# Kernel optimization log

Measured on AMD Instinct MI355X. Metric: run time of the kernel, lower is better.

The kernel has to match this reference:

```python
import jax, jax.numpy as jnp
import numpy as np

N = 50000       # nodes
E = 800000      # edges
IN = 128        # in_channels
HID = 64        # hidden_channels
OUT = 32        # out_channels
H = 4           # heads
EH = 64         # edge_hidden_channels
EOUT = 2        # edge_out_channels
NEG_SLOPE = 0.2 # PyG GATConv default


def gat_conv(x, edge_index, W, att_src, att_dst, bias, num_nodes):
    """PyG GATConv, concat=False, add_self_loops=False, eval mode (no dropout).
    edge_attr is ignored because edge_dim=None (lin_edge is None in PyG).
    Returns (out [N, C], alpha [E, H])."""
    heads, C = att_src.shape
    xl = (x @ W).reshape(-1, heads, C)                 # [N, H, C]
    src, dst = edge_index[0], edge_index[1]
    a_src = jnp.sum(xl * att_src, axis=-1)             # [N, H]
    a_dst = jnp.sum(xl * att_dst, axis=-1)             # [N, H]
    alpha = jax.nn.leaky_relu(a_src[src] + a_dst[dst], NEG_SLOPE)  # [E, H]
    # segment softmax over destination nodes
    amax = jax.ops.segment_max(alpha, dst, num_segments=num_nodes)
    amax = jnp.where(jnp.isfinite(amax), amax, 0.0)
    ex = jnp.exp(alpha - amax[dst])
    denom = jax.ops.segment_sum(ex, dst, num_segments=num_nodes)
    alpha_n = ex / (denom[dst] + 1e-16)                # [E, H]
    msg = xl[src] * alpha_n[:, :, None]                # [E, H, C]
    out = jax.ops.segment_sum(msg, dst, num_segments=num_nodes)  # [N, H, C]
    out = out.mean(axis=1) + bias                      # concat=False -> head mean
    return out, alpha_n


def setup_inputs() -> dict:
    key = jax.random.key(0)
    ks = jax.random.split(key, 16)
    x = jax.random.normal(ks[0], (N, IN), dtype=jnp.float32)
    edge_index = jax.random.randint(ks[1], (2, E), 0, N, dtype=jnp.int32)
    edge_attr = jax.random.normal(ks[2], (E, 5), dtype=jnp.float32)
    s = lambda fan: 1.0 / np.sqrt(fan)
    W1 = jax.random.normal(ks[3], (IN, H * HID), dtype=jnp.float32) * s(IN)
    att1_src = jax.random.normal(ks[4], (H, HID), dtype=jnp.float32) * s(HID)
    att1_dst = jax.random.normal(ks[5], (H, HID), dtype=jnp.float32) * s(HID)
    b1 = jnp.zeros((HID,), dtype=jnp.float32)
    W3 = jax.random.normal(ks[6], (HID, H * OUT), dtype=jnp.float32) * s(HID)
    att3_src = jax.random.normal(ks[7], (H, OUT), dtype=jnp.float32) * s(OUT)
    att3_dst = jax.random.normal(ks[8], (H, OUT), dtype=jnp.float32) * s(OUT)
    b3 = jnp.zeros((OUT,), dtype=jnp.float32)
    EIN = 2 * OUT + H  # cat(out_src, alpha, out_dst)
    mW1 = jax.random.normal(ks[9], (EIN, EH), dtype=jnp.float32) * s(EIN)
    mb1 = jnp.zeros((EH,), dtype=jnp.float32)
    mW2 = jax.random.normal(ks[10], (EH, EOUT), dtype=jnp.float32) * s(EH)
    mb2 = jnp.zeros((EOUT,), dtype=jnp.float32)
    return {"x": x, "edge_index": edge_index, "edge_attr": edge_attr,
            "return_attention_weights": 1,
            "W1": W1, "att1_src": att1_src, "att1_dst": att1_dst, "b1": b1,
            "W3": W3, "att3_src": att3_src, "att3_dst": att3_dst, "b3": b3,
            "mW1": mW1, "mb1": mb1, "mW2": mW2, "mb2": mb2}


def reference(x, edge_index, edge_attr, return_attention_weights,
              W1, att1_src, att1_dst, b1, W3, att3_src, att3_dst, b3,
              mW1, mb1, mW2, mb2):
    edge_len = edge_attr.shape[0]  # == E (no self loops added)
    out, alpha = gat_conv(x, edge_index, W1, att1_src, att1_dst, b1, N)
    out, alpha = gat_conv(out, edge_index, W3, att3_src, att3_dst, b3, N)
    # F.dropout with training=False is the identity (eval mode)
    ei = edge_index[:, :edge_len]
    al = alpha[:edge_len, :]
    out_src = out[ei[0]]                                # [E, OUT]
    out_dst = out[ei[1]]                                # [E, OUT]
    edge_feat = jnp.concatenate([out_src, al, out_dst], axis=-1)  # [E, 2*OUT+H]
    h = jax.nn.relu(edge_feat @ mW1 + mb1)
    edge_out = h @ mW2 + mb2                            # [E, EOUT]
    return (out, edge_out)
```

## Files before the change

### kernel.cpp

```cpp
#include <hip/hip_runtime.h>
#include <hip/hip_fp16.h>

constexpr int NN   = 50000;
constexpr int EE   = 800000;
constexpr int INF  = 128;
constexpr int NH   = 4;
constexpr int GR64 = (NN + 63) / 64;
constexpr int EB   = (EE + 255) / 256;
constexpr int NCH  = (NN + 255) / 256;

struct __align__(8) h4 { __half2 a, b; };

__device__ __forceinline__ float elw(float a) {
    a = (a > 0.f) ? a : 0.2f * a;
    return __expf(a);
}


template <int CH, bool HOUT>
__device__ __forceinline__ void gemm_att_tile48(const float* __restrict__ A,
                                                const float* __restrict__ B,
                                                void* __restrict__ Cv,
                                                const float* __restrict__ att_s,
                                                const float* __restrict__ att_d,
                                                float* __restrict__ a_s,
                                                float* __restrict__ a_d,
                                                int N, int K, int M,
                                                int row0, int col0, int tid,
                                                float (*As)[68], float (*Bs)[132]) {
    const int tx = tid & 15, ty = tid >> 4;
    float acc[4][8] = {};

    for (int k0 = 0; k0 < K; k0 += 32) {
        {
            const int a_row = tid >> 2;
            const int a_k   = (tid & 3) * 8;
            const int gr    = row0 + a_row;
            float4 v0 = make_float4(0.f,0.f,0.f,0.f), v1 = make_float4(0.f,0.f,0.f,0.f);
            if (gr < N) {
                const float* ap = A + (size_t)gr * K + k0 + a_k;
                v0 = *(const float4*)ap;
                v1 = *(const float4*)(ap + 4);
            }
            As[a_k + 0][a_row] = v0.x; As[a_k + 1][a_row] = v0.y;
            As[a_k + 2][a_row] = v0.z; As[a_k + 3][a_row] = v0.w;
            As[a_k + 4][a_row] = v1.x; As[a_k + 5][a_row] = v1.y;
            As[a_k + 6][a_row] = v1.z; As[a_k + 7][a_row] = v1.w;
        }
        {
            const int b_k = tid >> 4;
            const int b_c = (tid & 15) * 8;
            const float* bp0 = B + (size_t)(k0 + b_k) * M + col0 + b_c;
            const float* bp1 = B + (size_t)(k0 + b_k + 16) * M + col0 + b_c;
            *(float4*)&Bs[b_k][b_c]          = *(const float4*)bp0;
            *(float4*)&Bs[b_k][b_c + 4]      = *(const float4*)(bp0 + 4);
            *(float4*)&Bs[b_k + 16][b_c]     = *(const float4*)bp1;
            *(float4*)&Bs[b_k + 16][b_c + 4] = *(const float4*)(bp1 + 4);
        }
        __syncthreads();
        #pragma unroll
        for (int kk = 0; kk < 32; ++kk) {
            const float4 a  = *(const float4*)&As[kk][ty * 4];
            const float4 b0 = *(const float4*)&Bs[kk][tx * 4];
            const float4 b1 = *(const float4*)&Bs[kk][64 + tx * 4];
            const float av[4] = {a.x, a.y, a.z, a.w};
            const float bv[8] = {b0.x,b0.y,b0.z,b0.w,b1.x,b1.y,b1.z,b1.w};
            #pragma unroll
            for (int i = 0; i < 4; ++i)
                #pragma unroll
                for (int j = 0; j < 8; ++j)
                    acc[i][j] = fmaf(av[i], bv[j], acc[i][j]);
        }
        __syncthreads();
    }

    const int c0 = col0 + tx * 4;
    const int c1 = c0 + 64;
    const int head0 = c0 / CH, pos0 = c0 % CH;
    const int head1 = c1 / CH, pos1 = c1 % CH;
    float attS[8], attD[8];
    #pragma unroll
    for (int j = 0; j < 4; ++j) {
        attS[j]     = att_s[head0 * CH + pos0 + j];
        attD[j]     = att_d[head0 * CH + pos0 + j];
        attS[j + 4] = att_s[head1 * CH + pos1 + j];
        attD[j + 4] = att_d[head1 * CH + pos1 + j];
    }
    #pragma unroll
    for (int i = 0; i < 4; ++i) {
        const int r = row0 + ty * 4 + i;
        if (r < N) {
            if constexpr (HOUT) {
                __half* C = (__half*)Cv;
                __half* cp0 = C + (size_t)r * M + c0;
                __half* cp1 = C + (size_t)r * M + c1;
                *(__half2*)(cp0)     = __halves2half2(__float2half_rn(acc[i][0]), __float2half_rn(acc[i][1]));
                *(__half2*)(cp0 + 2) = __halves2half2(__float2half_rn(acc[i][2]), __float2half_rn(acc[i][3]));
                *(__half2*)(cp1)     = __halves2half2(__float2half_rn(acc[i][4]), __float2half_rn(acc[i][5]));
                *(__half2*)(cp1 + 2) = __halves2half2(__float2half_rn(acc[i][6]), __float2half_rn(acc[i][7]));
            } else {
                float* C = (float*)Cv;
                *(float4*)(C + (size_t)r * M + c0) = make_float4(acc[i][0], acc[i][1], acc[i][2], acc[i][3]);
                *(float4*)(C + (size_t)r * M + c1) = make_float4(acc[i][4], acc[i][5], acc[i][6], acc[i][7]);
            }
        }
        float ss0 = 0.f, sd0 = 0.f, ss1 = 0.f, sd1 = 0.f;
        #pragma unroll
        for (int j = 0; j < 4; ++j) {
            ss0 = fmaf(acc[i][j], attS[j], ss0);
            sd0 = fmaf(acc[i][j], attD[j], sd0);
            ss1 = fmaf(acc[i][j + 4], attS[j + 4], ss1);
            sd1 = fmaf(acc[i][j + 4], attD[j + 4], sd1);
        }
        #pragma unroll
        for (int msk = 1; msk < CH / 4; msk <<= 1) {
            ss0 += __shfl_xor(ss0, msk, 64);
            sd0 += __shfl_xor(sd0, msk, 64);
            ss1 += __shfl_xor(ss1, msk, 64);
            sd1 += __shfl_xor(sd1, msk, 64);
        }
        if ((tx & (CH / 4 - 1)) == 0 && r < N) {
            a_s[r * NH + head0] = ss0;
            a_d[r * NH + head0] = sd0;
            a_s[r * NH + head1] = ss1;
            a_d[r * NH + head1] = sd1;
        }
    }
}

__device__ __forceinline__ void gemm_pq_tile48(const float* __restrict__ A,
                                               const float* __restrict__ B,
                                               __half* __restrict__ C,
                                               int N, int K, int M,
                                               int row0, int col0, int tid,
                                               float (*As)[68], float (*Bs)[132]) {
    const int tx = tid & 15, ty = tid >> 4;
    float acc[4][8] = {};
    for (int k0 = 0; k0 < K; k0 += 32) {
        {
            const int a_row = tid >> 2;
            const int a_k   = (tid & 3) * 8;
            const int gr    = row0 + a_row;
            float4 v0 = make_float4(0.f,0.f,0.f,0.f), v1 = make_float4(0.f,0.f,0.f,0.f);
            if (gr < N) {
                const float* ap = A + (size_t)gr * K + k0 + a_k;
                v0 = *(const float4*)ap;
                v1 = *(const float4*)(ap + 4);
            }
            As[a_k + 0][a_row] = v0.x; As[a_k + 1][a_row] = v0.y;
            As[a_k + 2][a_row] = v0.z; As[a_k + 3][a_row] = v0.w;
            As[a_k + 4][a_row] = v1.x; As[a_k + 5][a_row] = v1.y;
            As[a_k + 6][a_row] = v1.z; As[a_k + 7][a_row] = v1.w;
        }
        {
            const int b_k = tid >> 4;
            const int b_c = (tid & 15) * 8;
            const float* bp0 = B + (size_t)(k0 + b_k) * M + col0 + b_c;
            const float* bp1 = B + (size_t)(k0 + b_k + 16) * M + col0 + b_c;
            *(float4*)&Bs[b_k][b_c]          = *(const float4*)bp0;
            *(float4*)&Bs[b_k][b_c + 4]      = *(const float4*)(bp0 + 4);
            *(float4*)&Bs[b_k + 16][b_c]     = *(const float4*)bp1;
            *(float4*)&Bs[b_k + 16][b_c + 4] = *(const float4*)(bp1 + 4);
        }
        __syncthreads();
        #pragma unroll
        for (int kk = 0; kk < 32; ++kk) {
            const float4 a  = *(const float4*)&As[kk][ty * 4];
            const float4 b0 = *(const float4*)&Bs[kk][tx * 4];
            const float4 b1 = *(const float4*)&Bs[kk][64 + tx * 4];
            const float av[4] = {a.x, a.y, a.z, a.w};
            const float bv[8] = {b0.x,b0.y,b0.z,b0.w,b1.x,b1.y,b1.z,b1.w};
            #pragma unroll
            for (int i = 0; i < 4; ++i)
                #pragma unroll
                for (int j = 0; j < 8; ++j)
                    acc[i][j] = fmaf(av[i], bv[j], acc[i][j]);
        }
        __syncthreads();
    }
    const int c0 = col0 + tx * 4;
    const int c1 = c0 + 64;
    #pragma unroll
    for (int i = 0; i < 4; ++i) {
        const int r = row0 + ty * 4 + i;
        if (r < N) {
            __half* cp0 = C + (size_t)r * M + c0;
            __half* cp1 = C + (size_t)r * M + c1;
            *(__half2*)(cp0)     = __halves2half2(__float2half_rn(acc[i][0]), __float2half_rn(acc[i][1]));
            *(__half2*)(cp0 + 2) = __halves2half2(__float2half_rn(acc[i][2]), __float2half_rn(acc[i][3]));
            *(__half2*)(cp1)     = __halves2half2(__float2half_rn(acc[i][4]), __float2half_rn(acc[i][5]));
            *(__half2*)(cp1 + 2) = __halves2half2(__float2half_rn(acc[i][6]), __float2half_rn(acc[i][7]));
        }
    }
}


__device__ __forceinline__ void softagg1_node(int n, int lane,
                                              const int* __restrict__ rowptr,
                                              const int* __restrict__ psrc,
                                              const float* __restrict__ a_s,
                                              const float* __restrict__ a_d,
                                              const __half* __restrict__ xl,
                                              const float* __restrict__ bias,
                                              float* __restrict__ out) {
    const int r0 = rowptr[n], r1 = rowptr[n + 1];
    const int hh = lane >> 4;
    const float ad = a_d[n * NH + hh];

    const h4* X = (const h4*)xl;
    float4 A0 = {0,0,0,0}, A1 = {0,0,0,0}, A2 = {0,0,0,0}, A3 = {0,0,0,0};
    float sum = 0.f;
    int j = r0;
    for (; j + 7 < r1; j += 8) {
        const int s0 = psrc[j],     s1 = psrc[j + 1], s2 = psrc[j + 2], s3 = psrc[j + 3];
        const int s4 = psrc[j + 4], s5 = psrc[j + 5], s6 = psrc[j + 6], s7 = psrc[j + 7];
        const float w0 = elw(a_s[s0 * NH + hh] + ad);
        const float w1 = elw(a_s[s1 * NH + hh] + ad);
        const float w2 = elw(a_s[s2 * NH + hh] + ad);
        const float w3 = elw(a_s[s3 * NH + hh] + ad);
        const float w4 = elw(a_s[s4 * NH + hh] + ad);
        const float w5 = elw(a_s[s5 * NH + hh] + ad);
        const float w6 = elw(a_s[s6 * NH + hh] + ad);
        const float w7 = elw(a_s[s7 * NH + hh] + ad);
        sum += ((w0 + w1) + (w2 + w3)) + ((w4 + w5) + (w6 + w7));
        const h4 v0 = X[(size_t)s0 * 64 + lane];
        const h4 v1 = X[(size_t)s1 * 64 + lane];
        const h4 v2 = X[(size_t)s2 * 64 + lane];
        const h4 v3 = X[(size_t)s3 * 64 + lane];
        const h4 v4 = X[(size_t)s4 * 64 + lane];
        const h4 v5 = X[(size_t)s5 * 64 + lane];
        const h4 v6 = X[(size_t)s6 * 64 + lane];
        const h4 v7 = X[(size_t)s7 * 64 + lane];
        float2 l0 = __half22float2(v0.a), m0 = __half22float2(v0.b);
        float2 l1 = __half22float2(v1.a), m1 = __half22float2(v1.b);
        float2 l2 = __half22float2(v2.a), m2 = __half22float2(v2.b);
        float2 l3 = __half22float2(v3.a), m3 = __half22float2(v3.b);
        float2 l4 = __half22float2(v4.a), m4 = __half22float2(v4.b);
        float2 l5 = __half22float2(v5.a), m5 = __half22float2(v5.b);
        float2 l6 = __half22float2(v6.a), m6 = __half22float2(v6.b);
        float2 l7 = __half22float2(v7.a), m7 = __half22float2(v7.b);
        A0.x = fmaf(w0, l0.x, A0.x); A0.y = fmaf(w0, l0.y, A0.y);
        A0.z = fmaf(w0, m0.x, A0.z); A0.w = fmaf(w0, m0.y, A0.w);
        A1.x = fmaf(w1, l1.x, A1.x); A1.y = fmaf(w1, l1.y, A1.y);
        A1.z = fmaf(w1, m1.x, A1.z); A1.w = fmaf(w1, m1.y, A1.w);
        A2.x = fmaf(w2, l2.x, A2.x); A2.y = fmaf(w2, l2.y, A2.y);
        A2.z = fmaf(w2, m2.x, A2.z); A2.w = fmaf(w2, m2.y, A2.w);
        A3.x = fmaf(w3, l3.x, A3.x); A3.y = fmaf(w3, l3.y, A3.y);
        A3.z = fmaf(w3, m3.x, A3.z); A3.w = fmaf(w3, m3.y, A3.w);
        A0.x = fmaf(w4, l4.x, A0.x); A0.y = fmaf(w4, l4.y, A0.y);
        A0.z = fmaf(w4, m4.x, A0.z); A0.w = fmaf(w4, m4.y, A0.w);
        A1.x = fmaf(w5, l5.x, A1.x); A1.y = fmaf(w5, l5.y, A1.y);
        A1.z = fmaf(w5, m5.x, A1.z); A1.w = fmaf(w5, m5.y, A1.w);
        A2.x = fmaf(w6, l6.x, A2.x); A2.y = fmaf(w6, l6.y, A2.y);
        A2.z = fmaf(w6, m6.x, A2.z); A2.w = fmaf(w6, m6.y, A2.w);
        A3.x = fmaf(w7, l7.x, A3.x); A3.y = fmaf(w7, l7.y, A3.y);
        A3.z = fmaf(w7, m7.x, A3.z); A3.w = fmaf(w7, m7.y, A3.w);
    }
    for (; j < r1; ++j) {
        const int s0 = psrc[j];
        const float w0 = elw(a_s[s0 * NH + hh] + ad);
        sum += w0;
        const h4 v0 = X[(size_t)s0 * 64 + lane];
        float2 l0 = __half22float2(v0.a), m0 = __half22float2(v0.b);
        A0.x = fmaf(w0, l0.x, A0.x); A0.y = fmaf(w0, l0.y, A0.y);
        A0.z = fmaf(w0, m0.x, A0.z); A0.w = fmaf(w0, m0.y, A0.w);
    }
    const float inv = 1.f / (sum + 1e-30f);
    float4 t;
    t.x = ((A0.x + A1.x) + (A2.x + A3.x)) * inv;
    t.y = ((A0.y + A1.y) + (A2.y + A3.y)) * inv;
    t.z = ((A0.z + A1.z) + (A2.z + A3.z)) * inv;
    t.w = ((A0.w + A1.w) + (A2.w + A3.w)) * inv;
    #pragma unroll
    for (int msk = 16; msk < 64; msk <<= 1) {
        t.x += __shfl_xor(t.x, msk, 64);
        t.y += __shfl_xor(t.y, msk, 64);
        t.z += __shfl_xor(t.z, msk, 64);
        t.w += __shfl_xor(t.w, msk, 64);
    }
    if (lane < 16) {
        const float4 b = ((const float4*)bias)[lane];
        float4 o;
        o.x = t.x * 0.25f + b.x; o.y = t.y * 0.25f + b.y;
        o.z = t.z * 0.25f + b.z; o.w = t.w * 0.25f + b.w;
        ((float4*)out)[(size_t)n * 16 + lane] = o;
    }
}

__device__ __forceinline__ void softagg2_node(int n, int lane,
                                              const int* __restrict__ rowptr,
                                              const int* __restrict__ psrc,
                                              const float* __restrict__ a_s,
                                              const float* __restrict__ a_d,
                                              float* __restrict__ alpha_p,
                                              float* __restrict__ inv_s,
                                              const __half* __restrict__ xl,
                                              const float* __restrict__ bias,
                                              float* __restrict__ out) {
    const int r0 = rowptr[n], r1 = rowptr[n + 1];
    const int cl = lane & 31, half = lane >> 5, hh = cl >> 3;
    const float ad = a_d[n * NH + hh];
    const bool writer = (cl & 7) == 0;

    const h4* X = (const h4*)xl;
    float4 A0 = {0,0,0,0}, A1 = {0,0,0,0};
    float sum = 0.f;
    int j = r0;
    for (; j + 7 < r1; j += 8) {
        const int ja = j + half, jc = j + 2 + half, je = j + 4 + half, jg = j + 6 + half;
        const int sa = psrc[ja], sc = psrc[jc], se = psrc[je], sg = psrc[jg];
        const float wa = elw(a_s[sa * NH + hh] + ad);
        const float wc = elw(a_s[sc * NH + hh] + ad);
        const float we = elw(a_s[se * NH + hh] + ad);
        const float wg = elw(a_s[sg * NH + hh] + ad);
        if (writer) {
            alpha_p[ja * NH + hh] = wa; alpha_p[jc * NH + hh] = wc;
            alpha_p[je * NH + hh] = we; alpha_p[jg * NH + hh] = wg;
        }
        sum += (wa + wc) + (we + wg);
        const h4 va = X[(size_t)sa * 32 + cl];
        const h4 vc = X[(size_t)sc * 32 + cl];
        const h4 ve = X[(size_t)se * 32 + cl];
        const h4 vg = X[(size_t)sg * 32 + cl];
        const float2 la = __half22float2(va.a), ma = __half22float2(va.b);
        const float2 lc = __half22float2(vc.a), mc = __half22float2(vc.b);
        const float2 le = __half22float2(ve.a), me = __half22float2(ve.b);
        const float2 lg = __half22float2(vg.a), mg = __half22float2(vg.b);
        A0.x = fmaf(wa, la.x, A0.x); A0.y = fmaf(wa, la.y, A0.y);
        A0.z = fmaf(wa, ma.x, A0.z); A0.w = fmaf(wa, ma.y, A0.w);
        A1.x = fmaf(wc, lc.x, A1.x); A1.y = fmaf(wc, lc.y, A1.y);
        A1.z = fmaf(wc, mc.x, A1.z); A1.w = fmaf(wc, mc.y, A1.w);
        A0.x = fmaf(we, le.x, A0.x); A0.y = fmaf(we, le.y, A0.y);
        A0.z = fmaf(we, me.x, A0.z); A0.w = fmaf(we, me.y, A0.w);
        A1.x = fmaf(wg, lg.x, A1.x); A1.y = fmaf(wg, lg.y, A1.y);
        A1.z = fmaf(wg, mg.x, A1.z); A1.w = fmaf(wg, mg.y, A1.w);
    }
    for (; j < r1; j += 2) {
        const int ja = j + half;
        const bool valid = ja < r1;
        const int sa = psrc[valid ? ja : r0];
        float wa = 0.f;
        if (valid) {
            wa = elw(a_s[sa * NH + hh] + ad);
            if (writer) alpha_p[ja * NH + hh] = wa;
        }
        sum += wa;
        const h4 va = X[(size_t)sa * 32 + cl];
        const float2 la = __half22float2(va.a), ma = __half22float2(va.b);
        A0.x = fmaf(wa, la.x, A0.x); A0.y = fmaf(wa, la.y, A0.y);
        A0.z = fmaf(wa, ma.x, A0.z); A0.w = fmaf(wa, ma.y, A0.w);
    }
    sum += __shfl_xor(sum, 32, 64);
    const float inv = 1.f / (sum + 1e-30f);
    if (writer && half == 0) inv_s[n * NH + hh] = inv;

    float4 t;
    t.x = A0.x + A1.x; t.y = A0.y + A1.y; t.z = A0.z + A1.z; t.w = A0.w + A1.w;
    t.x += __shfl_xor(t.x, 32, 64);
    t.y += __shfl_xor(t.y, 32, 64);
    t.z += __shfl_xor(t.z, 32, 64);
    t.w += __shfl_xor(t.w, 32, 64);
    t.x *= inv; t.y *= inv; t.z *= inv; t.w *= inv;
    #pragma unroll
    for (int q = 0; q < 2; ++q) {
        const int msk = (q == 0) ? 8 : 16;
        t.x += __shfl_xor(t.x, msk, 64);
        t.y += __shfl_xor(t.y, msk, 64);
        t.z += __shfl_xor(t.z, msk, 64);
        t.w += __shfl_xor(t.w, msk, 64);
    }
    if (lane < 8) {
        const float4 b = ((const float4*)bias)[lane];
        float4 o;
        o.x = t.x * 0.25f + b.x; o.y = t.y * 0.25f + b.y;
        o.z = t.z * 0.25f + b.z; o.w = t.w * 0.25f + b.w;
        ((float4*)out)[(size_t)n * 8 + lane] = o;
    }
}


__global__ __launch_bounds__(256) void count_deg_k(const int* __restrict__ ei,
                                                   int* __restrict__ deg) {
    const int e = blockIdx.x * 256 + threadIdx.x;
    if (e < EE) atomicAdd(&deg[ei[EE + e]], 1);
}

__global__ __launch_bounds__(256) void pack_w1_k(const float* __restrict__ mW1,
                                                 float* __restrict__ W1pq) {
    const int idx = blockIdx.x * 256 + threadIdx.x;
    if (idx >= 32 * 128) return;
    const int k = idx >> 7, j = idx & 127;
    W1pq[idx] = (j < 64) ? mW1[k * 64 + j] : mW1[(36 + k) * 64 + (j - 64)];
}

template <int CH, bool HOUT>
__global__ __launch_bounds__(256) void gemm_att48_k(const float* __restrict__ A,
                                                    const float* __restrict__ B,
                                                    void* __restrict__ Cv,
                                                    const float* __restrict__ att_s,
                                                    const float* __restrict__ att_d,
                                                    float* __restrict__ a_s,
                                                    float* __restrict__ a_d,
                                                    int N, int K, int M) {
    __shared__ float As[32][68];
    __shared__ float Bs[32][132];
    gemm_att_tile48<CH, HOUT>(A, B, Cv, att_s, att_d, a_s, a_d, N, K, M,
                              blockIdx.x * 64, blockIdx.y * 128, threadIdx.x, As, Bs);
}

__global__ __launch_bounds__(256) void gemm_pq48_k(const float* __restrict__ A,
                                                   const float* __restrict__ B,
                                                   __half* __restrict__ C,
                                                   int N, int K, int M) {
    __shared__ float As[32][68];
    __shared__ float Bs[32][132];
    gemm_pq_tile48(A, B, C, N, K, M, blockIdx.x * 64, blockIdx.y * 128, threadIdx.x, As, Bs);
}

__global__ __launch_bounds__(256) void scan1_k(const int* __restrict__ deg,
                                               int* __restrict__ bsum) {
    __shared__ int sw[4];
    const int tid = threadIdx.x, lane = tid & 63, wv = tid >> 6;
    const int i = blockIdx.x * 256 + tid;
    int s = (i < NN) ? deg[i] : 0;
    #pragma unroll
    for (int d = 1; d < 64; d <<= 1) s += __shfl_xor(s, d, 64);
    if (lane == 0) sw[wv] = s;
    __syncthreads();
    if (tid == 0) bsum[blockIdx.x] = sw[0] + sw[1] + sw[2] + sw[3];
}

__global__ __launch_bounds__(256) void scan2_k(const int* __restrict__ bsum,
                                               int* __restrict__ boff) {
    __shared__ int sw[8];
    const int tid = threadIdx.x, lane = tid & 63, wv = tid >> 6;
    int v = (tid < NCH) ? bsum[tid] : 0;
    int incl = v;
    #pragma unroll
    for (int d = 1; d < 64; d <<= 1) {
        int t = __shfl_up(incl, d, 64);
        if (lane >= d) incl += t;
    }
    if (lane == 63) sw[wv] = incl;
    __syncthreads();
    if (wv == 0 && lane < 4) {
        int s4 = sw[lane];
        #pragma unroll
        for (int d = 1; d < 4; d <<= 1) {
            int t = __shfl_up(s4, d, 64);
            if (lane >= d) s4 += t;
        }
        sw[lane + 4] = s4;
    }
    __syncthreads();
    const int woff = (wv > 0) ? sw[wv - 1 + 4] : 0;
    if (tid < NCH) boff[tid] = woff + incl - v;
}

__global__ __launch_bounds__(256) void scan3_k(const int* __restrict__ deg,
                                               const int* __restrict__ boff,
                                               int* __restrict__ rowptr,
                                               int* __restrict__ cursor) {
    __shared__ int sw[8];
    const int tid = threadIdx.x, lane = tid & 63, wv = tid >> 6;
    const int c = blockIdx.x;
    const int i = c * 256 + tid;
    int v = (i < NN) ? deg[i] : 0;
    int incl = v;
    #pragma unroll
    for (int d = 1; d < 64; d <<= 1) {
        int t = __shfl_up(incl, d, 64);
        if (lane >= d) incl += t;
    }
    if (lane == 63) sw[wv] = incl;
    __syncthreads();
    if (wv == 0 && lane < 4) {
        int s4 = sw[lane];
        #pragma unroll
        for (int d = 1; d < 4; d <<= 1) {
            int t = __shfl_up(s4, d, 64);
            if (lane >= d) s4 += t;
        }
        sw[lane + 4] = s4;
    }
    __syncthreads();
    const int excl = boff[c] + ((wv > 0) ? sw[wv - 1 + 4] : 0) + incl - v;
    if (i < NN) { rowptr[i] = excl; cursor[i] = excl; }
    if (c == 0 && tid == 0) rowptr[NN] = EE;
}

__global__ __launch_bounds__(256) void scatter_perm_k(const int* __restrict__ ei,
                                                      int* __restrict__ cursor,
                                                      int* __restrict__ perm,
                                                      int* __restrict__ psrc,
                                                      int* __restrict__ pdst) {
    const int e = blockIdx.x * 256 + threadIdx.x;
    if (e >= EE) return;
    const int d = ei[EE + e];
    const int p = atomicAdd(&cursor[d], 1);
    perm[p] = e;
    psrc[p] = ei[e];
    pdst[p] = d;
}

__global__ __launch_bounds__(256) void softagg1h_k(const int* __restrict__ rowptr,
                                                   const int* __restrict__ psrc,
                                                   const float* __restrict__ a_s,
                                                   const float* __restrict__ a_d,
                                                   const __half* __restrict__ xl,
                                                   const float* __restrict__ bias,
                                                   float* __restrict__ out) {
    const int n = blockIdx.x * 4 + (threadIdx.x >> 6);
    if (n >= NN) return;
    softagg1_node(n, threadIdx.x & 63, rowptr, psrc, a_s, a_d, xl, bias, out);
}

__global__ __launch_bounds__(256) void softagg2h_k(const int* __restrict__ rowptr,
                                                   const int* __restrict__ psrc,
                                                   const float* __restrict__ a_s,
                                                   const float* __restrict__ a_d,
                                                   float* __restrict__ alpha_p,
                                                   float* __restrict__ inv_s,
                                                   const __half* __restrict__ xl,
                                                   const float* __restrict__ bias,
                                                   float* __restrict__ out) {
    const int n = blockIdx.x * 4 + (threadIdx.x >> 6);
    if (n >= NN) return;
    softagg2_node(n, threadIdx.x & 63, rowptr, psrc, a_s, a_d, alpha_p, inv_s, xl, bias, out);
}

__global__ __launch_bounds__(256) void edge_mlp_k(const __half* __restrict__ PQ,
                                                  const float* __restrict__ alpha_p,
                                                  const float* __restrict__ inv_s,
                                                  const int* __restrict__ psrc,
                                                  const int* __restrict__ pdst,
                                                  const int* __restrict__ perm,
                                                  const float* __restrict__ mW1,
                                                  const float* __restrict__ mb1,
                                                  const float* __restrict__ mW2,
                                                  const float* __restrict__ mb2,
                                                  float* __restrict__ out) {
    const int lane = threadIdx.x & 63, wvv = threadIdx.x >> 6;
    const int g = lane >> 4, c = lane & 15;

    const float4 wa0 = *(const float4*)&mW1[32 * 64 + c * 4];
    const float4 wa1 = *(const float4*)&mW1[33 * 64 + c * 4];
    const float4 wa2 = *(const float4*)&mW1[34 * 64 + c * 4];
    const float4 wa3 = *(const float4*)&mW1[35 * 64 + c * 4];
    const float4 b1v = *(const float4*)&mb1[c * 4];
    const float4 w2a = *(const float4*)&mW2[c * 8];
    const float4 w2b = *(const float4*)&mW2[c * 8 + 4];
    const float bo0 = mb2[0], bo1 = mb2[1];

    const h4* PQ4 = (const h4*)PQ;
    const int gw = blockIdx.x * 4 + wvv;
    const int stride4 = gridDim.x * 4 * 4;

    for (int jb = gw * 4; jb < EE; jb += stride4) {
        const int j = jb + g;
        const int s = psrc[j];
        const int d = pdst[j];
        const float4 ar = *(const float4*)&alpha_p[(size_t)j * 4];
        const float4 iv = *(const float4*)&inv_s[(size_t)d * 4];
        const float al0 = ar.x * iv.x, al1 = ar.y * iv.y;
        const float al2 = ar.z * iv.z, al3 = ar.w * iv.w;
        const h4 ph = PQ4[(size_t)s * 32 + c];
        const h4 qh = PQ4[(size_t)d * 32 + 16 + c];
        const float2 pl = __half22float2(ph.a), pm = __half22float2(ph.b);
        const float2 ql = __half22float2(qh.a), qm = __half22float2(qh.b);
        float4 h;
        h.x = pl.x + ql.x + b1v.x; h.y = pl.y + ql.y + b1v.y;
        h.z = pm.x + qm.x + b1v.z; h.w = pm.y + qm.y + b1v.w;
        h.x = fmaf(al0, wa0.x, h.x); h.y = fmaf(al0, wa0.y, h.y);
        h.z = fmaf(al0, wa0.z, h.z); h.w = fmaf(al0, wa0.w, h.w);
        h.x = fmaf(al1, wa1.x, h.x); h.y = fmaf(al1, wa1.y, h.y);
        h.z = fmaf(al1, wa1.z, h.z); h.w = fmaf(al1, wa1.w, h.w);
        h.x = fmaf(al2, wa2.x, h.x); h.y = fmaf(al2, wa2.y, h.y);
        h.z = fmaf(al2, wa2.z, h.z); h.w = fmaf(al2, wa2.w, h.w);
        h.x = fmaf(al3, wa3.x, h.x); h.y = fmaf(al3, wa3.y, h.y);
        h.z = fmaf(al3, wa3.z, h.z); h.w = fmaf(al3, wa3.w, h.w);
        h.x = fmaxf(h.x, 0.f); h.y = fmaxf(h.y, 0.f);
        h.z = fmaxf(h.z, 0.f); h.w = fmaxf(h.w, 0.f);

        float v0 = h.x * w2a.x + h.y * w2a.z + h.z * w2b.x + h.w * w2b.z;
        float v1 = h.x * w2a.y + h.y * w2a.w + h.z * w2b.y + h.w * w2b.w;
        #pragma unroll
        for (int msk = 1; msk < 16; msk <<= 1) {
            v0 += __shfl_xor(v0, msk, 64);
            v1 += __shfl_xor(v1, msk, 64);
        }
        if (c == 0)
            *(float2*)&out[(size_t)perm[j] * 2] = make_float2(v0 + bo0, v1 + bo1);
    }
}

extern "C" void kernel_launch(void* const* d_in, const int* in_sizes, int n_in,
                              void* d_out, int out_size, void* d_ws, size_t ws_size,
                              hipStream_t stream) {
    const float* x        = (const float*)d_in[0];
    const int*   ei       = (const int*)d_in[1];
    const float* W1       = (const float*)d_in[4];
    const float* att1_src = (const float*)d_in[5];
    const float* att1_dst = (const float*)d_in[6];
    const float* b1       = (const float*)d_in[7];
    const float* W3       = (const float*)d_in[8];
    const float* att3_src = (const float*)d_in[9];
    const float* att3_dst = (const float*)d_in[10];
    const float* b3       = (const float*)d_in[11];
    const float* mW1      = (const float*)d_in[12];
    const float* mb1      = (const float*)d_in[13];
    const float* mW2      = (const float*)d_in[14];
    const float* mb2      = (const float*)d_in[15];

    float* out_nodes = (float*)d_out;
    float* out_edges = out_nodes + (size_t)NN * 32;

    float* ws = (float*)d_ws;
    __half*   xlh     = (__half*)ws;
    __half*   xl2h    = (__half*)ws;
    __half*   PQh     = (__half*)ws;
    float*    h1      = ws + 12800000;
    float*    alpha_p = ws + 16000000;
    float*    a_s     = ws + 25600000;
    float*    a_d     = ws + 25800000;
    float*    W1pq    = ws + 26000000;
    float*    inv_s   = ws + 26100000;
    int*      bsum    = (int*)(ws + 26300000);
    int*      boff    = (int*)(ws + 26301000);
    int*      deg     = (int*)(ws + 26400000);
    int*      cursor  = (int*)(ws + 26450000);
    int*      rowptr  = (int*)(ws + 26500000);
    int*      perm    = (int*)(ws + 26550008);
    int*      psrc    = (int*)(ws + 27350008);
    int*      pdst    = (int*)(ws + 28150008);

    const int NB4 = (NN + 3) / 4;

    hipMemsetAsync(deg, 0, (size_t)NN * 4, stream);
    count_deg_k<<<EB, 256, 0, stream>>>(ei, deg);
    pack_w1_k<<<16, 256, 0, stream>>>(mW1, W1pq);
    gemm_att48_k<64, true><<<dim3(GR64, 2), 256, 0, stream>>>(x, W1, xlh,
                                                              att1_src, att1_dst,
                                                              a_s, a_d, NN, INF, NH * 64);
    scan1_k<<<NCH, 256, 0, stream>>>(deg, bsum);
    scan2_k<<<1, 256, 0, stream>>>(bsum, boff);
    scan3_k<<<NCH, 256, 0, stream>>>(deg, boff, rowptr, cursor);
    scatter_perm_k<<<EB, 256, 0, stream>>>(ei, cursor, perm, psrc, pdst);
    softagg1h_k<<<NB4, 256, 0, stream>>>(rowptr, psrc, a_s, a_d, xlh, b1, h1);
    gemm_att48_k<32, true><<<dim3(GR64, 1), 256, 0, stream>>>(h1, W3, xl2h,
                                                              att3_src, att3_dst,
                                                              a_s, a_d, NN, 64, NH * 32);
    softagg2h_k<<<NB4, 256, 0, stream>>>(rowptr, psrc, a_s, a_d, alpha_p, inv_s, xl2h, b3,
                                         out_nodes);
    gemm_pq48_k<<<dim3(GR64, 1), 256, 0, stream>>>(out_nodes, W1pq, PQh, NN, 32, 128);
    edge_mlp_k<<<2048, 256, 0, stream>>>(PQh, alpha_p, inv_s, psrc, pdst, perm,
                                         mW1, mb1, mW2, mb2, out_edges);
}
```

Baseline: 450.0 us.

## Replace first-layer GEMM with split-bf16 MFMA kernel fused with attention scores

```diff
diff --git a/kernel.cpp b/kernel.cpp
--- a/kernel.cpp
+++ b/kernel.cpp
@@ -11,11 +11,140 @@
 
 struct __align__(8) h4 { __half2 a, b; };
 
+typedef short bf16x8 __attribute__((ext_vector_type(8)));
+typedef float f32x4v __attribute__((ext_vector_type(4)));
+
 __device__ __forceinline__ float elw(float a) {
     a = (a > 0.f) ? a : 0.2f * a;
     return __expf(a);
 }
 
+__device__ __forceinline__ short bf16_hi(float x) {
+    return (short)(__float_as_uint(x) >> 16);
+}
+__device__ __forceinline__ float bf16_back(short h) {
+    return __uint_as_float(((unsigned)(unsigned short)h) << 16);
+}
+
+__global__ __launch_bounds__(256) void gemm1_mfma_k(const float* __restrict__ A,
+                                                    const float* __restrict__ B,
+                                                    __half* __restrict__ C,
+                                                    const float* __restrict__ att_s,
+                                                    const float* __restrict__ att_d,
+                                                    float* __restrict__ a_s,
+                                                    float* __restrict__ a_d) {
+    __shared__ short Ah[64][72], Al[64][72];
+    __shared__ short Bh[64][72], Bl[64][72];
+    const int tid  = threadIdx.x;
+    const int lane = tid & 63, w = tid >> 6;
+    const int row0 = blockIdx.x * 64;
+    const int head = blockIdx.y;
+    const int c0   = head * 64;
+
+    const int rl = lane & 15, gq = lane >> 4;
+
+    f32x4v acc0 = {0,0,0,0}, acc1 = {0,0,0,0}, acc2 = {0,0,0,0}, acc3 = {0,0,0,0};
+
+    for (int ks = 0; ks < 2; ++ks) {
+        {
+            const int ar = tid >> 2;
+            const int kb = (tid & 3) * 4;
+            const int grow = row0 + ar;
+            #pragma unroll
+            for (int pass = 0; pass < 4; ++pass) {
+                const int kl = kb + pass * 16;
+                float4 v = make_float4(0.f, 0.f, 0.f, 0.f);
+                if (grow < NN) v = *(const float4*)(A + (size_t)grow * 128 + ks * 64 + kl);
+                short4 hi, lo;
+                hi.x = bf16_hi(v.x); lo.x = bf16_hi(v.x - bf16_back(hi.x));
+                hi.y = bf16_hi(v.y); lo.y = bf16_hi(v.y - bf16_back(hi.y));
+                hi.z = bf16_hi(v.z); lo.z = bf16_hi(v.z - bf16_back(hi.z));
+                hi.w = bf16_hi(v.w); lo.w = bf16_hi(v.w - bf16_back(hi.w));
+                *(short4*)&Ah[ar][kl] = hi;
+                *(short4*)&Al[ar][kl] = lo;
+            }
+        }
+        {
+            const int c  = lane;
+            const int kb = w * 16;
+            #pragma unroll
+            for (int chunk = 0; chunk < 2; ++chunk) {
+                short hi8[8], lo8[8];
+                #pragma unroll
+                for (int i = 0; i < 8; ++i) {
+                    const int kl = kb + chunk * 8 + i;
+                    const float v = B[(size_t)(ks * 64 + kl) * 256 + c0 + c];
+                    hi8[i] = bf16_hi(v);
+                    lo8[i] = bf16_hi(v - bf16_back(hi8[i]));
+                }
+                *(bf16x8*)&Bh[c][kb + chunk * 8] =
+                    (bf16x8){hi8[0],hi8[1],hi8[2],hi8[3],hi8[4],hi8[5],hi8[6],hi8[7]};
+                *(bf16x8*)&Bl[c][kb + chunk * 8] =
+                    (bf16x8){lo8[0],lo8[1],lo8[2],lo8[3],lo8[4],lo8[5],lo8[6],lo8[7]};
+            }
+        }
+        __syncthreads();
+
+        bf16x8 aH0 = *(const bf16x8*)&Ah[w * 16 + rl][gq * 8];
+        bf16x8 aH1 = *(const bf16x8*)&Ah[w * 16 + rl][32 + gq * 8];
+        bf16x8 aL0 = *(const bf16x8*)&Al[w * 16 + rl][gq * 8];
+        bf16x8 aL1 = *(const bf16x8*)&Al[w * 16 + rl][32 + gq * 8];
+
+        #pragma unroll
+        for (int cf = 0; cf < 4; ++cf) {
+            const int bc = cf * 16 + rl;
+            bf16x8 bH0 = *(const bf16x8*)&Bh[bc][gq * 8];
+            bf16x8 bH1 = *(const bf16x8*)&Bh[bc][32 + gq * 8];
+            bf16x8 bL0 = *(const bf16x8*)&Bl[bc][gq * 8];
+            bf16x8 bL1 = *(const bf16x8*)&Bl[bc][32 + gq * 8];
+            f32x4v t = (cf == 0) ? acc0 : (cf == 1) ? acc1 : (cf == 2) ? acc2 : acc3;
+            t = __builtin_amdgcn_mfma_f32_16x16x32_bf16(aH0, bH0, t, 0, 0, 0);
+            t = __builtin_amdgcn_mfma_f32_16x16x32_bf16(aL0, bH0, t, 0, 0, 0);
+            t = __builtin_amdgcn_mfma_f32_16x16x32_bf16(aH0, bL0, t, 0, 0, 0);
+            t = __builtin_amdgcn_mfma_f32_16x16x32_bf16(aH1, bH1, t, 0, 0, 0);
+            t = __builtin_amdgcn_mfma_f32_16x16x32_bf16(aL1, bH1, t, 0, 0, 0);
+            t = __builtin_amdgcn_mfma_f32_16x16x32_bf16(aH1, bL1, t, 0, 0, 0);
+            if (cf == 0) acc0 = t; else if (cf == 1) acc1 = t;
+            else if (cf == 2) acc2 = t; else acc3 = t;
+        }
+        __syncthreads();
+    }
+
+    float sS[4] = {0.f, 0.f, 0.f, 0.f};
+    float sD[4] = {0.f, 0.f, 0.f, 0.f};
+    #pragma unroll
+    for (int cf = 0; cf < 4; ++cf) {
+        const f32x4v t = (cf == 0) ? acc0 : (cf == 1) ? acc1 : (cf == 2) ? acc2 : acc3;
+        const int gcol = c0 + cf * 16 + rl;
+        const float atS = att_s[gcol];
+        const float atD = att_d[gcol];
+        #pragma unroll
+        for (int r = 0; r < 4; ++r) {
+            const int grow = row0 + w * 16 + gq * 4 + r;
+            if (grow < NN) C[(size_t)grow * 256 + gcol] = __float2half_rn(t[r]);
+            sS[r] = fmaf(t[r], atS, sS[r]);
+            sD[r] = fmaf(t[r], atD, sD[r]);
+        }
+    }
+    #pragma unroll
+    for (int r = 0; r < 4; ++r) {
+        #pragma unroll
+        for (int msk = 1; msk < 16; msk <<= 1) {
+            sS[r] += __shfl_xor(sS[r], msk, 64);
+            sD[r] += __shfl_xor(sD[r], msk, 64);
+        }
+    }
+    if (rl == 0) {
+        #pragma unroll
+        for (int r = 0; r < 4; ++r) {
+            const int grow = row0 + w * 16 + gq * 4 + r;
+            if (grow < NN) {
+                a_s[grow * NH + head] = sS[r];
+                a_d[grow * NH + head] = sD[r];
+            }
+        }
+    }
+}
 
 template <int CH, bool HOUT>
 __device__ __forceinline__ void gemm_att_tile48(const float* __restrict__ A,
@@ -639,9 +768,8 @@
     hipMemsetAsync(deg, 0, (size_t)NN * 4, stream);
     count_deg_k<<<EB, 256, 0, stream>>>(ei, deg);
     pack_w1_k<<<16, 256, 0, stream>>>(mW1, W1pq);
-    gemm_att48_k<64, true><<<dim3(GR64, 2), 256, 0, stream>>>(x, W1, xlh,
-                                                              att1_src, att1_dst,
-                                                              a_s, a_d, NN, INF, NH * 64);
+    gemm1_mfma_k<<<dim3(GR64, 4), 256, 0, stream>>>(x, W1, xlh, att1_src, att1_dst,
+                                                    a_s, a_d);
     scan1_k<<<NCH, 256, 0, stream>>>(deg, bsum);
     scan2_k<<<1, 256, 0, stream>>>(bsum, boff);
     scan3_k<<<NCH, 256, 0, stream>>>(deg, boff, rowptr, cursor);
```

Measured after the change: 426.9 us. 1.05x faster.
